# Kernel optimization log

Measured on AMD Instinct MI355X. Metric: run time of the kernel, lower is better.

Reference implementation:

```python
import jax, jax.numpy as jnp
import numpy as np

NUM_HEADS = 16
HEAD_DIM = 32  # dim=512 / num_heads=16


def _rel_pos_bias(table, index, window_area):
    # table: [(2W-1)^2, H], index: [N, N] int -> bias [1, H, N, N]
    bias = table[index.reshape(-1)].reshape(window_area, window_area, -1)
    return jnp.transpose(bias, (2, 0, 1))[None]


def setup_inputs() -> dict:
    key = jax.random.key(0)
    ks = jax.random.split(key, 6)
    B, N, C = 256, 196, 512
    x = jax.random.normal(ks[0], (B, N, C), dtype=jnp.float32)
    qkv_w = jax.random.normal(ks[1], (3 * C, C), dtype=jnp.float32) * 0.02
    proj_w = jax.random.normal(ks[2], (C, C), dtype=jnp.float32) * 0.02
    proj_b = jax.random.normal(ks[3], (C,), dtype=jnp.float32) * 0.02
    rel_pos_bias_table = jax.random.normal(ks[4], (729, NUM_HEADS), dtype=jnp.float32) * 0.02
    rel_pos_index = jax.random.randint(ks[5], (N, N), 0, 729, dtype=jnp.int64)
    return {
        "x": x,
        "qkv_w": qkv_w,
        "proj_w": proj_w,
        "proj_b": proj_b,
        "rel_pos_bias_table": rel_pos_bias_table,
        "rel_pos_index": rel_pos_index,
        "window_area": N,
    }


def reference(x, qkv_w, proj_w, proj_b, rel_pos_bias_table, rel_pos_index, window_area):
    B, N, C = x.shape
    H, hd = NUM_HEADS, HEAD_DIM
    scale = hd ** -0.5
    # qkv projection (no bias), split into q,k,v: [B, H, N, hd]
    qkv = (x @ qkv_w.T).reshape(B, N, 3, H, hd)
    qkv = jnp.transpose(qkv, (2, 0, 3, 1, 4))
    q, k, v = qkv[0], qkv[1], qkv[2]
    attn = jnp.einsum("bhnd,bhmd->bhnm", q * scale, k)
    attn = attn + _rel_pos_bias(rel_pos_bias_table, rel_pos_index, window_area)
    attn = jax.nn.softmax(attn, axis=-1)
    out = jnp.einsum("bhnm,bhmd->bhnd", attn, v)
    out = jnp.transpose(out, (0, 2, 1, 3)).reshape(B, N, C)
    return out @ proj_w.T + proj_b
```

## Files before the change

kernel.cpp:

```cpp
#include <hip/hip_runtime.h>
#include <hip/hip_bf16.h>


typedef unsigned short u16;
typedef unsigned int u32;
typedef __attribute__((ext_vector_type(8))) short bf16x8;
typedef __attribute__((ext_vector_type(4))) float f32x4;

__device__ __forceinline__ u16 f2bf(float f) {
  union { float f; unsigned u; } c; c.f = f;
  unsigned r = ((c.u >> 16) & 1u) + 0x7fffu;
  return (u16)((c.u + r) >> 16);
}

__global__ __launch_bounds__(256) void cvt_f32_bf16(const float* __restrict__ in,
                                                    u16* __restrict__ out, int n) {
  int i = (blockIdx.x * 256 + threadIdx.x) * 4;
  if (i >= n) return;
  float4 v = *(const float4*)(in + i);
  ushort4 o;
  o.x = f2bf(v.x); o.y = f2bf(v.y); o.z = f2bf(v.z); o.w = f2bf(v.w);
  *(ushort4*)(out + i) = o;
}

__global__ __launch_bounds__(256) void zero_vt_pad(u16* __restrict__ vt) {
  int i = blockIdx.x * 256 + threadIdx.x;
  if (i >= 4096 * 32 * 36) return;
  int row = i / 36, c = i - row * 36;
  vt[row * 232 + 196 + c] = 0;
}

__global__ __launch_bounds__(256) void build_bias(const float* __restrict__ table,
                                                  const int* __restrict__ idx,
                                                  float* __restrict__ outb) {
  int e = blockIdx.x * 256 + threadIdx.x;
  int r = e & 3, lane = (e >> 2) & 63, rest = e >> 8;
  int mt = rest % 14; rest /= 14;
  int nt = rest % 13; int h = rest / 13;
  int n = nt * 16 + (lane & 15);
  int m = mt * 16 + ((lane >> 4) << 2) + r;
  float v;
  if (m < 196) {
    int nc = n < 196 ? n : 195;
    v = table[idx[nc * 196 + m] * 16 + h];
  } else {
    v = -1e30f;
  }
  outb[e] = v;
}

template<int EPI>
__global__ __launch_bounds__(256) void gemm_bt(
    const u16* __restrict__ A, const u16* __restrict__ Bt,
    u16* __restrict__ q, u16* __restrict__ kk, u16* __restrict__ vt,
    const float* __restrict__ pbias, float* __restrict__ out) {
  constexpr int K = 512;
  constexpr int NWGX = (EPI == 0) ? 12 : 4;
  constexpr int NWG = NWGX * 392;
  __shared__ u16 As[2][128 * 32];
  __shared__ u16 Bs[2][128 * 32];
  int d = blockIdx.y * NWGX + blockIdx.x;
  int nf = (d & 7) * (NWG >> 3) + (d >> 3);
  const int bx = nf / NWGX;
  const int by = nf - bx * NWGX;
  const int tid = threadIdx.x;
  const int w = tid >> 6, l = tid & 63;
  const int wm = (w >> 1) * 64, wn = (w & 1) * 64;
  const int lr = l & 15, lg = l >> 4;
  const int lk = (lg ^ (lr & 3)) * 8;
  const int qg = ((l & 3) ^ ((l >> 2) & 3)) * 8;
  f32x4 acc[4][4] = {};

  const u16* ga0 = A + (long)(bx * 128 + w * 16 + (l >> 2)) * K + qg;
  const u16* gb0 = Bt + (long)(by * 128 + w * 16 + (l >> 2)) * K + qg;

#define STAGE(nb, kt)                                                          \
  {                                                                            \
    const u16* ga = ga0 + (kt) * 32;                                           \
    const u16* gb = gb0 + (kt) * 32;                                           \
    __builtin_amdgcn_global_load_lds((const __attribute__((address_space(1))) void*)ga, \
        (__attribute__((address_space(3))) void*)&As[nb][w * 512], 16, 0, 0);  \
    __builtin_amdgcn_global_load_lds((const __attribute__((address_space(1))) void*)(ga + 64 * K), \
        (__attribute__((address_space(3))) void*)&As[nb][2048 + w * 512], 16, 0, 0); \
    __builtin_amdgcn_global_load_lds((const __attribute__((address_space(1))) void*)gb, \
        (__attribute__((address_space(3))) void*)&Bs[nb][w * 512], 16, 0, 0);  \
    __builtin_amdgcn_global_load_lds((const __attribute__((address_space(1))) void*)(gb + 64 * K), \
        (__attribute__((address_space(3))) void*)&Bs[nb][2048 + w * 512], 16, 0, 0); \
  }

  STAGE(0, 0);
  __syncthreads();
  for (int kt = 0; kt < 16; ++kt) {
    const int cur = kt & 1;
    if (kt < 15) STAGE(cur ^ 1, kt + 1);
    bf16x8 a[4], b[4];
#pragma unroll
    for (int i = 0; i < 4; ++i)
      a[i] = *(const bf16x8*)&As[cur][(wm + i * 16 + lr) * 32 + lk];
#pragma unroll
    for (int j = 0; j < 4; ++j)
      b[j] = *(const bf16x8*)&Bs[cur][(wn + j * 16 + lr) * 32 + lk];
#pragma unroll
    for (int i = 0; i < 4; ++i)
#pragma unroll
      for (int j = 0; j < 4; ++j)
        acc[i][j] = __builtin_amdgcn_mfma_f32_16x16x32_bf16(a[i], b[j], acc[i][j], 0, 0, 0);
    __syncthreads();
  }
#undef STAGE

  const int colbase = by * 128 + wn;
  const int rowbase = bx * 128 + wm;
#pragma unroll
  for (int i = 0; i < 4; ++i) {
    const int row0 = rowbase + i * 16 + (l >> 4) * 4;
    const int bb = row0 / 196;
    const int nn0 = row0 - bb * 196;
#pragma unroll
    for (int j = 0; j < 4; ++j) {
      const int col = colbase + j * 16 + lr;
      if (EPI == 0) {
        const int t = col >> 9, h = (col >> 5) & 15, dd = col & 31;
        const long bh = (long)bb * 16 + h;
        if (t == 0) {
          const float s = 0.17677669529663687f;
#pragma unroll
          for (int r = 0; r < 4; ++r)
            q[(bh * 196 + nn0 + r) * 32 + dd] = f2bf(acc[i][j][r] * s);
        } else if (t == 1) {
#pragma unroll
          for (int r = 0; r < 4; ++r)
            kk[(bh * 196 + nn0 + r) * 32 + dd] = f2bf(acc[i][j][r]);
        } else {
          ushort4 pv;
          pv.x = f2bf(acc[i][j][0]); pv.y = f2bf(acc[i][j][1]);
          pv.z = f2bf(acc[i][j][2]); pv.w = f2bf(acc[i][j][3]);
          *(ushort4*)&vt[(bh * 32 + dd) * 232 + nn0] = pv;
        }
      } else {
        const float pb = pbias[col];
#pragma unroll
        for (int r = 0; r < 4; ++r)
          out[(long)(row0 + r) * 512 + col] = acc[i][j][r] + pb;
      }
    }
  }
}

__global__ __launch_bounds__(256, 4) void attn_kernel(
    const u16* __restrict__ q, const u16* __restrict__ kk,
    const u16* __restrict__ vt, const float* __restrict__ biasA,
    u16* __restrict__ ao) {
  __shared__ u16 Ks[196 * 40];
  __shared__ u16 Vs[32 * 232];
  const int bhd = blockIdx.x;
  const int h = bhd >> 8, bb = bhd & 255;
  const int bh = bb * 16 + h;
  const int tid = threadIdx.x, w = tid >> 6, l = tid & 63;
  const int lr = l & 15, lg = l >> 4;

  {
    const u16* kg = kk + (long)bh * (196 * 32);
#pragma unroll
    for (int p = 0; p < 4; ++p) {
      int m = p * 64 + (tid >> 2);
      if (m < 196) {
        int c = (tid & 3) * 8;
        *(bf16x8*)&Ks[m * 40 + c] = *(const bf16x8*)(kg + m * 32 + c);
      }
    }
    const u16* vg = vt + (long)bh * (32 * 232);
#pragma unroll
    for (int p = 0; p < 4; ++p) {
      int off = (p * 256 + tid) * 8;
      if (off < 32 * 232) *(bf16x8*)&Vs[off] = *(const bf16x8*)(vg + off);
    }
  }
  __syncthreads();

  const float* biasH = biasA + (long)h * (13 * 14 * 256);
  const int sA = ((l & 16) << 1) + lr;
  const int sB = sA + 16;
  const bool hi = (l & 32) != 0;

  for (int nt = w; nt < 13; nt += 4) {
    int nq = nt * 16 + lr; if (nq > 195) nq = 195;
    bf16x8 qa = *(const bf16x8*)(q + ((long)bh * 196 + nq) * 32 + lg * 8);

    u32 pk[14][2];
    float ssum = 0.f;
#pragma unroll
    for (int mt = 0; mt < 14; ++mt) {
      int row = mt * 16 + lr; if (row > 195) row = 195;
      bf16x8 kb = *(const bf16x8*)&Ks[row * 40 + lg * 8];
      const float4 b4 = *(const float4*)(biasH + ((nt * 14 + mt) * 64 + l) * 4);
      f32x4 c; c[0] = b4.x; c[1] = b4.y; c[2] = b4.z; c[3] = b4.w;
      f32x4 S = __builtin_amdgcn_mfma_f32_16x16x32_bf16(kb, qa, c, 0, 0, 0);
      float e0 = __expf(S[0]), e1 = __expf(S[1]);
      float e2 = __expf(S[2]), e3 = __expf(S[3]);
      ssum += (e0 + e1) + (e2 + e3);
      asm("v_cvt_pk_bf16_f32 %0, %1, %2" : "=v"(pk[mt][0]) : "v"(e0), "v"(e1));
      asm("v_cvt_pk_bf16_f32 %0, %1, %2" : "=v"(pk[mt][1]) : "v"(e2), "v"(e3));
    }
    ssum += __shfl_xor(ssum, 16);
    ssum += __shfl_xor(ssum, 32);
    float invT = __builtin_amdgcn_rcpf(ssum);

    f32x4 O0 = {}, O1 = {};
#pragma unroll
    for (int ks = 0; ks < 7; ++ks) {
      u32 a0 = (u32)__shfl((int)pk[2 * ks][0], sA);
      u32 a1 = (u32)__shfl((int)pk[2 * ks][1], sA);
      u32 a2 = (u32)__shfl((int)pk[2 * ks][0], sB);
      u32 a3 = (u32)__shfl((int)pk[2 * ks][1], sB);
      u32 c0 = (u32)__shfl((int)pk[2 * ks + 1][0], sA);
      u32 c1 = (u32)__shfl((int)pk[2 * ks + 1][1], sA);
      u32 c2 = (u32)__shfl((int)pk[2 * ks + 1][0], sB);
      u32 c3 = (u32)__shfl((int)pk[2 * ks + 1][1], sB);
      bf16x8 pa;
      ((u32*)&pa)[0] = hi ? c0 : a0;
      ((u32*)&pa)[1] = hi ? c1 : a1;
      ((u32*)&pa)[2] = hi ? c2 : a2;
      ((u32*)&pa)[3] = hi ? c3 : a3;
      bf16x8 v0 = *(const bf16x8*)&Vs[lr * 232 + ks * 32 + lg * 8];
      bf16x8 v1 = *(const bf16x8*)&Vs[(16 + lr) * 232 + ks * 32 + lg * 8];
      O0 = __builtin_amdgcn_mfma_f32_16x16x32_bf16(pa, v0, O0, 0, 0, 0);
      O1 = __builtin_amdgcn_mfma_f32_16x16x32_bf16(pa, v1, O1, 0, 0, 0);
    }

    float inv[4];
#pragma unroll
    for (int r = 0; r < 4; ++r) inv[r] = __shfl(invT, lg * 4 + r);
    const int nr0 = nt * 16 + lg * 4;
#pragma unroll
    for (int r = 0; r < 4; ++r) {
      int nr = nr0 + r;
      if (nr < 196) {
        long base = ((long)bb * 196 + nr) * 512 + h * 32;
        ao[base + lr] = f2bf(O0[r] * inv[r]);
        ao[base + 16 + lr] = f2bf(O1[r] * inv[r]);
      }
    }
  }
}

extern "C" void kernel_launch(void* const* d_in, const int* in_sizes, int n_in,
                              void* d_out, int out_size, void* d_ws, size_t ws_size,
                              hipStream_t stream) {
  const float* x      = (const float*)d_in[0];
  const float* qkv_w  = (const float*)d_in[1];
  const float* proj_w = (const float*)d_in[2];
  const float* proj_b = (const float*)d_in[3];
  const float* table  = (const float*)d_in[4];
  const int*   ridx   = (const int*)d_in[5];
  float* out = (float*)d_out;

  char* ws = (char*)d_ws;
  u16*   xb    = (u16*)(ws);
  u16*   qwb   = (u16*)(ws + 51380224);
  u16*   pwb   = (u16*)(ws + 52953088);
  u16*   qb    = (u16*)(ws + 53477376);
  u16*   kb    = (u16*)(ws + 104857600);
  u16*   vtb   = (u16*)(ws + 156237824);
  float* biasA = (float*)(ws + 217055232);

  cvt_f32_bf16<<<25088, 256, 0, stream>>>(x, xb, 25690112);
  cvt_f32_bf16<<<768, 256, 0, stream>>>(qkv_w, qwb, 786432);
  cvt_f32_bf16<<<256, 256, 0, stream>>>(proj_w, pwb, 262144);
  build_bias<<<2912, 256, 0, stream>>>(table, ridx, biasA);
  zero_vt_pad<<<18432, 256, 0, stream>>>(vtb);

  gemm_bt<0><<<dim3(12, 392), 256, 0, stream>>>(xb, qwb, qb, kb, vtb, nullptr, nullptr);
  attn_kernel<<<4096, 256, 0, stream>>>(qb, kb, vtb, biasA, xb );
  gemm_bt<1><<<dim3(4, 392), 256, 0, stream>>>(xb, pwb, nullptr, nullptr, nullptr, proj_b, out);
}
```

Before: 284.5 us.

## Replace 128x128 GEMM with 256x256 tile, 4-stage LDS pipeline and 8 waves

Both projection GEMMs move from 128x128 tiles with 4 waves and double buffering to 256x256 tiles with 8 waves and a 4-slot LDS ring. A and B loads are split across two half-iterations, with explicit vmcnt waits, raw barriers and s_setprio around the MFMA blocks. The aim is more data reuse per tile and more global-to-LDS latency hidden behind compute. In exchange it uses more LDS (128KB) and registers per block, and tail iterations reload the clamped last k-tile.

```diff
diff --git a/kernel.cpp b/kernel.cpp
--- a/kernel.cpp
+++ b/kernel.cpp
@@ -50,75 +50,107 @@
 }
 
 template<int EPI>
-__global__ __launch_bounds__(256) void gemm_bt(
+__global__ __launch_bounds__(512, 2) void gemm256(
     const u16* __restrict__ A, const u16* __restrict__ Bt,
     u16* __restrict__ q, u16* __restrict__ kk, u16* __restrict__ vt,
     const float* __restrict__ pbias, float* __restrict__ out) {
   constexpr int K = 512;
-  constexpr int NWGX = (EPI == 0) ? 12 : 4;
-  constexpr int NWG = NWGX * 392;
-  __shared__ u16 As[2][128 * 32];
-  __shared__ u16 Bs[2][128 * 32];
-  int d = blockIdx.y * NWGX + blockIdx.x;
-  int nf = (d & 7) * (NWG >> 3) + (d >> 3);
-  const int bx = nf / NWGX;
-  const int by = nf - bx * NWGX;
+  constexpr int NWGX = (EPI == 0) ? 6 : 2;
+  constexpr int NWG = NWGX * 196;
+  __shared__ u16 LA[4][8192];
+  __shared__ u16 LB[4][8192];
+
+  int id = blockIdx.y * NWGX + blockIdx.x;
+  int nf = (id & 7) * (NWG >> 3) + (id >> 3);
+  const int bx = nf / NWGX, by = nf - (nf / NWGX) * NWGX;
+
   const int tid = threadIdx.x;
   const int w = tid >> 6, l = tid & 63;
-  const int wm = (w >> 1) * 64, wn = (w & 1) * 64;
   const int lr = l & 15, lg = l >> 4;
-  const int lk = (lg ^ (lr & 3)) * 8;
-  const int qg = ((l & 3) ^ ((l >> 2) & 3)) * 8;
-  f32x4 acc[4][4] = {};
-
-  const u16* ga0 = A + (long)(bx * 128 + w * 16 + (l >> 2)) * K + qg;
-  const u16* gb0 = Bt + (long)(by * 128 + w * 16 + (l >> 2)) * K + qg;
-
-#define STAGE(nb, kt)                                                          \
-  {                                                                            \
-    const u16* ga = ga0 + (kt) * 32;                                           \
-    const u16* gb = gb0 + (kt) * 32;                                           \
-    __builtin_amdgcn_global_load_lds((const __attribute__((address_space(1))) void*)ga, \
-        (__attribute__((address_space(3))) void*)&As[nb][w * 512], 16, 0, 0);  \
-    __builtin_amdgcn_global_load_lds((const __attribute__((address_space(1))) void*)(ga + 64 * K), \
-        (__attribute__((address_space(3))) void*)&As[nb][2048 + w * 512], 16, 0, 0); \
-    __builtin_amdgcn_global_load_lds((const __attribute__((address_space(1))) void*)gb, \
-        (__attribute__((address_space(3))) void*)&Bs[nb][w * 512], 16, 0, 0);  \
-    __builtin_amdgcn_global_load_lds((const __attribute__((address_space(1))) void*)(gb + 64 * K), \
-        (__attribute__((address_space(3))) void*)&Bs[nb][2048 + w * 512], 16, 0, 0); \
-  }
-
-  STAGE(0, 0);
-  __syncthreads();
+  const int wm = w >> 2, wn = w & 3;
+
+  const int gq = (l & 3) ^ ((l >> 3) & 3);
+  const u16* gA = A + (long)(bx * 256 + w * 32 + (l >> 2)) * K + gq * 8;
+  const u16* gB = Bt + (long)(by * 256 + w * 32 + (l >> 2)) * K + gq * 8;
+
+  const int swz = (lg ^ ((lr >> 1) & 3)) * 8;
+  const int ra = (wm * 128 + lr) * 32 + swz;
+  const int rb = (wn * 64 + lr) * 32 + swz;
+
+#define STAGE_A(st, kt)                                                        \
+  __builtin_amdgcn_global_load_lds((const __attribute__((address_space(1))) void*)(gA + (kt) * 32), \
+      (__attribute__((address_space(3))) void*)&LA[st][w * 1024], 16, 0, 0);   \
+  __builtin_amdgcn_global_load_lds((const __attribute__((address_space(1))) void*)(gA + 16 * K + (kt) * 32), \
+      (__attribute__((address_space(3))) void*)&LA[st][w * 1024 + 512], 16, 0, 0);
+#define STAGE_B(st, kt)                                                        \
+  __builtin_amdgcn_global_load_lds((const __attribute__((address_space(1))) void*)(gB + (kt) * 32), \
+      (__attribute__((address_space(3))) void*)&LB[st][w * 1024], 16, 0, 0);   \
+  __builtin_amdgcn_global_load_lds((const __attribute__((address_space(1))) void*)(gB + 16 * K + (kt) * 32), \
+      (__attribute__((address_space(3))) void*)&LB[st][w * 1024 + 512], 16, 0, 0);
+
+  f32x4 acc[8][4] = {};
+  bf16x8 bfr[4];
+
+  STAGE_A(0, 0); STAGE_B(0, 0);
+  STAGE_A(1, 1); STAGE_B(1, 1);
+  STAGE_A(2, 2); STAGE_B(2, 2);
+  asm volatile("s_waitcnt vmcnt(8)" ::: "memory");
+  __builtin_amdgcn_s_barrier();
+
   for (int kt = 0; kt < 16; ++kt) {
-    const int cur = kt & 1;
-    if (kt < 15) STAGE(cur ^ 1, kt + 1);
-    bf16x8 a[4], b[4];
-#pragma unroll
-    for (int i = 0; i < 4; ++i)
-      a[i] = *(const bf16x8*)&As[cur][(wm + i * 16 + lr) * 32 + lk];
-#pragma unroll
-    for (int j = 0; j < 4; ++j)
-      b[j] = *(const bf16x8*)&Bs[cur][(wn + j * 16 + lr) * 32 + lk];
-#pragma unroll
-    for (int i = 0; i < 4; ++i)
-#pragma unroll
-      for (int j = 0; j < 4; ++j)
-        acc[i][j] = __builtin_amdgcn_mfma_f32_16x16x32_bf16(a[i], b[j], acc[i][j], 0, 0, 0);
-    __syncthreads();
-  }
-#undef STAGE
-
-  const int colbase = by * 128 + wn;
-  const int rowbase = bx * 128 + wm;
-#pragma unroll
-  for (int i = 0; i < 4; ++i) {
-    const int row0 = rowbase + i * 16 + (l >> 4) * 4;
+    const int slot = kt & 3;
+    const int st = (kt + 3) & 3;
+    const int sk = (kt + 3 < 16) ? kt + 3 : 15;
+    const u16* as = &LA[slot][0];
+    const u16* bs = &LB[slot][0];
+
+    bf16x8 afr[4];
+#pragma unroll
+    for (int f = 0; f < 4; ++f) afr[f] = *(const bf16x8*)&as[ra + f * 512];
+#pragma unroll
+    for (int j2 = 0; j2 < 4; ++j2) bfr[j2] = *(const bf16x8*)&bs[rb + j2 * 512];
+    STAGE_A(st, sk);
+    asm volatile("s_waitcnt vmcnt(8)" ::: "memory");
+    __builtin_amdgcn_s_barrier();
+    asm volatile("s_waitcnt lgkmcnt(0)" ::: "memory");
+    __builtin_amdgcn_s_setprio(1);
+#pragma unroll
+    for (int f = 0; f < 4; ++f)
+#pragma unroll
+      for (int j2 = 0; j2 < 4; ++j2)
+        acc[f][j2] = __builtin_amdgcn_mfma_f32_16x16x32_bf16(afr[f], bfr[j2], acc[f][j2], 0, 0, 0);
+    __builtin_amdgcn_s_setprio(0);
+    __builtin_amdgcn_s_barrier();
+
+#pragma unroll
+    for (int f = 0; f < 4; ++f) afr[f] = *(const bf16x8*)&as[ra + (f + 4) * 512];
+    STAGE_B(st, sk);
+    asm volatile("s_waitcnt vmcnt(8)" ::: "memory");
+    __builtin_amdgcn_s_barrier();
+    asm volatile("s_waitcnt lgkmcnt(0)" ::: "memory");
+    __builtin_amdgcn_s_setprio(1);
+#pragma unroll
+    for (int f = 0; f < 4; ++f)
+#pragma unroll
+      for (int j2 = 0; j2 < 4; ++j2)
+        acc[f + 4][j2] = __builtin_amdgcn_mfma_f32_16x16x32_bf16(afr[f], bfr[j2], acc[f + 4][j2], 0, 0, 0);
+    __builtin_amdgcn_s_setprio(0);
+    __builtin_amdgcn_s_barrier();
+  }
+#undef STAGE_A
+#undef STAGE_B
+  asm volatile("s_waitcnt vmcnt(0)" ::: "memory");
+
+  const int colbase = by * 256 + wn * 64;
+  const int rowb = bx * 256 + wm * 128 + lg * 4;
+#pragma unroll
+  for (int f = 0; f < 8; ++f) {
+    const int row0 = rowb + f * 16;
     const int bb = row0 / 196;
     const int nn0 = row0 - bb * 196;
 #pragma unroll
-    for (int j = 0; j < 4; ++j) {
-      const int col = colbase + j * 16 + lr;
+    for (int j2 = 0; j2 < 4; ++j2) {
+      const int col = colbase + j2 * 16 + lr;
       if (EPI == 0) {
         const int t = col >> 9, h = (col >> 5) & 15, dd = col & 31;
         const long bh = (long)bb * 16 + h;
@@ -126,22 +158,22 @@
           const float s = 0.17677669529663687f;
 #pragma unroll
           for (int r = 0; r < 4; ++r)
-            q[(bh * 196 + nn0 + r) * 32 + dd] = f2bf(acc[i][j][r] * s);
+            q[(bh * 196 + nn0 + r) * 32 + dd] = f2bf(acc[f][j2][r] * s);
         } else if (t == 1) {
 #pragma unroll
           for (int r = 0; r < 4; ++r)
-            kk[(bh * 196 + nn0 + r) * 32 + dd] = f2bf(acc[i][j][r]);
+            kk[(bh * 196 + nn0 + r) * 32 + dd] = f2bf(acc[f][j2][r]);
         } else {
           ushort4 pv;
-          pv.x = f2bf(acc[i][j][0]); pv.y = f2bf(acc[i][j][1]);
-          pv.z = f2bf(acc[i][j][2]); pv.w = f2bf(acc[i][j][3]);
+          pv.x = f2bf(acc[f][j2][0]); pv.y = f2bf(acc[f][j2][1]);
+          pv.z = f2bf(acc[f][j2][2]); pv.w = f2bf(acc[f][j2][3]);
           *(ushort4*)&vt[(bh * 32 + dd) * 232 + nn0] = pv;
         }
       } else {
         const float pb = pbias[col];
 #pragma unroll
         for (int r = 0; r < 4; ++r)
-          out[(long)(row0 + r) * 512 + col] = acc[i][j][r] + pb;
+          out[(long)(row0 + r) * 512 + col] = acc[f][j2][r] + pb;
       }
     }
   }
@@ -270,7 +302,7 @@
   build_bias<<<2912, 256, 0, stream>>>(table, ridx, biasA);
   zero_vt_pad<<<18432, 256, 0, stream>>>(vtb);
 
-  gemm_bt<0><<<dim3(12, 392), 256, 0, stream>>>(xb, qwb, qb, kb, vtb, nullptr, nullptr);
+  gemm256<0><<<dim3(6, 196), 512, 0, stream>>>(xb, qwb, qb, kb, vtb, nullptr, nullptr);
   attn_kernel<<<4096, 256, 0, stream>>>(qb, kb, vtb, biasA, xb );
-  gemm_bt<1><<<dim3(4, 392), 256, 0, stream>>>(xb, pwb, nullptr, nullptr, nullptr, proj_b, out);
-}
+  gemm256<1><<<dim3(2, 196), 512, 0, stream>>>(xb, pwb, nullptr, nullptr, nullptr, proj_b, out);
+}
```

Result: slower. 295.9 us (+4.0%).
